# Kernel optimization log

Measured on AMD Instinct MI355X. Metric: run time of the kernel, lower is better.

## Reference

```python
import jax, jax.numpy as jnp
import numpy as np

KV_SIZE = 512


def setup_inputs() -> dict:
    key = jax.random.key(0)
    k1, k2, k3 = jax.random.split(key, 3)
    B, T, C = 8, 4096, 1024
    x = jax.random.normal(k1, (B, T, C), dtype=jnp.float32)
    k_t_1 = jax.random.normal(k2, (B, KV_SIZE, C), dtype=jnp.float32)
    v_t_1 = jax.random.normal(k3, (B, KV_SIZE, C), dtype=jnp.float32)
    return {"x": x, "k_t_1": k_t_1, "v_t_1": v_t_1}


def reference(x, k_t_1, v_t_1):
    # x: [B, T, C]; latent state k_t_1, v_t_1: [B, S=512, C]
    B, T, C = x.shape
    scale = 1.0 / jnp.sqrt(jnp.asarray(C, dtype=x.dtype))

    # Read: queries (tokens) attend over the fixed-size latent KV state.
    scores = jnp.einsum("btc,bsc->bts", x, k_t_1) * scale      # [B, T, S]
    att = jnp.einsum("bts,bsc->btc", jax.nn.softmax(scores, axis=-1), v_t_1)

    # Update: each latent slot attends over the incoming tokens and
    # accumulates the summary into the state (fixed-size KV cache update).
    k_scores = jnp.einsum("bsc,btc->bst", k_t_1, x) * scale     # [B, S, T]
    k_t = k_t_1 + jnp.einsum("bst,btc->bsc", jax.nn.softmax(k_scores, axis=-1), x)
    v_scores = jnp.einsum("bsc,btc->bst", v_t_1, x) * scale     # [B, S, T]
    v_t = v_t_1 + jnp.einsum("bst,btc->bsc", jax.nn.softmax(v_scores, axis=-1), x)

    return att, k_t, v_t
```

## Files before the change

### kernel.cpp

```cpp
#include <hip/hip_runtime.h>
#include <hip/hip_bf16.h>

#define BB 8
#define TT 4096
#define CC 1024
#define SS 512

typedef __bf16 bf16x8 __attribute__((ext_vector_type(8)));
typedef float f32x4 __attribute__((ext_vector_type(4)));
typedef unsigned short u16x8 __attribute__((ext_vector_type(8)));

__device__ __forceinline__ float bf2f(unsigned short u) {
  union { unsigned int i; float f; } x; x.i = ((unsigned int)u) << 16; return x.f;
}
__device__ __forceinline__ unsigned short f2bf(float f) {
  __hip_bfloat16 h = __float2bfloat16(f);
  unsigned short u; __builtin_memcpy(&u, &h, 2); return u;
}

__global__ void cvt_transpose(const float* __restrict__ in,
                              unsigned short* __restrict__ out_rm,
                              unsigned short* __restrict__ out_t,
                              int R, int Cd) {
  __shared__ float tile[64][65];
  const long bo = (long)blockIdx.z * R * Cd;
  const int r0 = blockIdx.x * 64, c0 = blockIdx.y * 64;
  const int tx = threadIdx.x, ty = threadIdx.y;
#pragma unroll
  for (int i = 0; i < 16; ++i) {
    int r = ty + i * 4;
    float v = in[bo + (long)(r0 + r) * Cd + c0 + tx];
    tile[r][tx] = v;
    out_rm[bo + (long)(r0 + r) * Cd + c0 + tx] = f2bf(v);
  }
  if (out_t != nullptr) {
    __syncthreads();
#pragma unroll
    for (int i = 0; i < 16; ++i) {
      int c = ty + i * 4;
      out_t[bo + (long)(c0 + c) * R + r0 + tx] = f2bf(tile[tx][c]);
    }
  }
}

__global__ void transpose_bf16(const unsigned short* __restrict__ in,
                               unsigned short* __restrict__ out,
                               int Rin, int Cin) {
  __shared__ unsigned short tile[64][72];
  const long bo = (long)blockIdx.z * Rin * Cin;
  const int r0 = blockIdx.x * 64, c0 = blockIdx.y * 64;
  const int tid = threadIdx.x;
  const int lr = tid >> 3;
  const int lc = (tid & 7) * 8;
#pragma unroll
  for (int p = 0; p < 2; ++p) {
    int r = lr + p * 32;
    *(u16x8*)&tile[r][lc] = *(const u16x8*)&in[bo + (long)(r0 + r) * Cin + c0 + lc];
  }
  __syncthreads();
#pragma unroll
  for (int p = 0; p < 2; ++p) {
    int s = lr + p * 32;
    u16x8 val;
#pragma unroll
    for (int j = 0; j < 8; ++j) val[j] = tile[lc + j][s];
    *(u16x8*)&out[bo + (long)(c0 + s) * Rin + r0 + lc] = val;
  }
}

template <int ROWLEN>
__global__ __launch_bounds__(256) void row_softmax(unsigned short* __restrict__ sc) {
  constexpr int NV = ROWLEN / 512;
  const int lane = threadIdx.x & 63;
  const long row = (long)blockIdx.x * 4 + (threadIdx.x >> 6);
  unsigned short* base = sc + row * (long)ROWLEN;
  u16x8 d[NV];
  float m = -1e30f;
#pragma unroll
  for (int v = 0; v < NV; ++v) {
    d[v] = *(const u16x8*)&base[(v * 64 + lane) * 8];
#pragma unroll
    for (int j = 0; j < 8; ++j) m = fmaxf(m, bf2f(d[v][j]));
  }
#pragma unroll
  for (int off = 32; off >= 1; off >>= 1) m = fmaxf(m, __shfl_xor(m, off, 64));
  float l = 0.f;
#pragma unroll
  for (int v = 0; v < NV; ++v) {
#pragma unroll
    for (int j = 0; j < 8; ++j) {
      float e = __expf(bf2f(d[v][j]) - m);
      l += e;
      d[v][j] = f2bf(e);
    }
  }
#pragma unroll
  for (int off = 32; off >= 1; off >>= 1) l += __shfl_xor(l, off, 64);
  const float inv = 1.f / l;
#pragma unroll
  for (int v = 0; v < NV; ++v) {
    u16x8 o;
#pragma unroll
    for (int j = 0; j < 8; ++j) o[j] = f2bf(bf2f(d[v][j]) * inv);
    *(u16x8*)&base[(v * 64 + lane) * 8] = o;
  }
}

template <bool OUT_BF16, bool RESID>
__global__ __launch_bounds__(256) void gemm_bt(
    const unsigned short* __restrict__ A, int lda, long sA,
    const unsigned short* __restrict__ Bt, int ldb, long sB,
    void* __restrict__ Cout, int ldc, long sC,
    const float* __restrict__ resid, long sR,
    float alpha, int M, int N, int K) {
  __shared__ unsigned short As[128 * 64];
  __shared__ unsigned short Bs[128 * 64];
  const int zb = blockIdx.z;
  const unsigned short* Ab = A + (long)zb * sA;
  const unsigned short* Bb = Bt + (long)zb * sB;
  const int m0 = blockIdx.y * 128;
  const int n0 = blockIdx.x * 128;
  const int tid = threadIdx.x;
  const int lane = tid & 63;
  const int wm = (tid >> 6) & 1;
  const int wn = tid >> 7;
  const int srow = tid >> 3;
  const int scol = (tid & 7) * 8;
  f32x4 zero = {0.f, 0.f, 0.f, 0.f};
  f32x4 acc[4][4];
#pragma unroll
  for (int i = 0; i < 4; ++i)
#pragma unroll
    for (int j = 0; j < 4; ++j) acc[i][j] = zero;

  for (int k0 = 0; k0 < K; k0 += 64) {
#pragma unroll
    for (int p = 0; p < 4; ++p) {
      int r = srow + p * 32;
      const unsigned short* g = Ab + (long)(m0 + r) * lda + k0 + scol;
      __builtin_amdgcn_global_load_lds(
          (const __attribute__((address_space(1))) void*)g,
          (__attribute__((address_space(3))) void*)&As[r * 64 + scol], 16, 0, 0);
    }
#pragma unroll
    for (int p = 0; p < 4; ++p) {
      int r = srow + p * 32;
      const unsigned short* g = Bb + (long)(n0 + r) * ldb + k0 + scol;
      __builtin_amdgcn_global_load_lds(
          (const __attribute__((address_space(1))) void*)g,
          (__attribute__((address_space(3))) void*)&Bs[r * 64 + scol], 16, 0, 0);
    }
    __syncthreads();
#pragma unroll
    for (int kk = 0; kk < 2; ++kk) {
      const int kof = kk * 32 + (lane >> 4) * 8;
      bf16x8 af[4], bfr[4];
#pragma unroll
      for (int i = 0; i < 4; ++i)
        af[i] = *(const bf16x8*)&As[(wm * 64 + i * 16 + (lane & 15)) * 64 + kof];
#pragma unroll
      for (int j = 0; j < 4; ++j)
        bfr[j] = *(const bf16x8*)&Bs[(wn * 64 + j * 16 + (lane & 15)) * 64 + kof];
#pragma unroll
      for (int i = 0; i < 4; ++i)
#pragma unroll
        for (int j = 0; j < 4; ++j)
          acc[i][j] = __builtin_amdgcn_mfma_f32_16x16x32_bf16(af[i], bfr[j], acc[i][j], 0, 0, 0);
    }
    __syncthreads();
  }
  const int rbase = (lane >> 4) * 4;
  const int cl = lane & 15;
#pragma unroll
  for (int i = 0; i < 4; ++i)
#pragma unroll
    for (int j = 0; j < 4; ++j)
#pragma unroll
      for (int r = 0; r < 4; ++r) {
        int row = m0 + wm * 64 + i * 16 + rbase + r;
        int col = n0 + wn * 64 + j * 16 + cl;
        long idx = (long)row * ldc + col;
        float v = acc[i][j][r] * alpha;
        if (RESID) v += resid[(long)zb * sR + idx];
        if (OUT_BF16)
          ((unsigned short*)Cout)[(long)zb * sC + idx] = f2bf(v);
        else
          ((float*)Cout)[(long)zb * sC + idx] = v;
      }
}

extern "C" void kernel_launch(void* const* d_in, const int* in_sizes, int n_in,
                              void* d_out, int out_size, void* d_ws, size_t ws_size,
                              hipStream_t stream) {
  const float* x = (const float*)d_in[0];
  const float* kin = (const float*)d_in[1];
  const float* vin = (const float*)d_in[2];

  float* att = (float*)d_out;
  float* kt = att + (long)BB * TT * CC;
  float* vt = kt + (long)BB * SS * CC;

  unsigned short* xb = (unsigned short*)d_out;
  unsigned short* xT = xb + (long)BB * TT * CC;

  char* w = (char*)d_ws;
  unsigned short* kb = (unsigned short*)w; w += (long)BB * SS * CC * 2;
  unsigned short* vb = (unsigned short*)w; w += (long)BB * SS * CC * 2;
  unsigned short* vT = (unsigned short*)w; w += (long)BB * CC * SS * 2;
  unsigned short* sc = (unsigned short*)w; w += (long)BB * TT * SS * 2;
  unsigned short* pk = (unsigned short*)w; w += (long)BB * SS * TT * 2;

  const float scale = 0.03125f;
  dim3 cblk(64, 4);

  cvt_transpose<<<dim3(TT / 64, CC / 64, BB), cblk, 0, stream>>>(x, xb, xT, TT, CC);
  cvt_transpose<<<dim3(SS / 64, CC / 64, BB), cblk, 0, stream>>>(kin, kb, (unsigned short*)nullptr, SS, CC);
  cvt_transpose<<<dim3(SS / 64, CC / 64, BB), cblk, 0, stream>>>(vin, vb, vT, SS, CC);

  gemm_bt<true, false><<<dim3(SS / 128, TT / 128, BB), 256, 0, stream>>>(
      xb, CC, (long)TT * CC, kb, CC, (long)SS * CC, sc, SS, (long)TT * SS,
      nullptr, 0, scale, TT, SS, CC);

  transpose_bf16<<<dim3(TT / 64, SS / 64, BB), 256, 0, stream>>>(sc, pk, TT, SS);
  row_softmax<TT><<<BB * SS / 4, 256, 0, stream>>>(pk);

  gemm_bt<false, true><<<dim3(CC / 128, SS / 128, BB), 256, 0, stream>>>(
      pk, TT, (long)SS * TT, xT, TT, (long)CC * TT, kt, CC, (long)SS * CC,
      kin, (long)SS * CC, 1.f, SS, CC, TT);

  row_softmax<SS><<<BB * TT / 4, 256, 0, stream>>>(sc);

  gemm_bt<true, false><<<dim3(TT / 128, SS / 128, BB), 256, 0, stream>>>(
      vb, CC, (long)SS * CC, xb, CC, (long)TT * CC, pk, TT, (long)SS * TT,
      nullptr, 0, scale, SS, TT, CC);
  row_softmax<TT><<<BB * SS / 4, 256, 0, stream>>>(pk);

  gemm_bt<false, true><<<dim3(CC / 128, SS / 128, BB), 256, 0, stream>>>(
      pk, TT, (long)SS * TT, xT, TT, (long)CC * TT, vt, CC, (long)SS * CC,
      vin, (long)SS * CC, 1.f, SS, CC, TT);

  gemm_bt<false, false><<<dim3(CC / 128, TT / 128, BB), 256, 0, stream>>>(
      sc, SS, (long)TT * SS, vT, SS, (long)CC * SS, att, CC, (long)TT * CC,
      nullptr, 0, 1.f, TT, CC, SS);
}
```

Measured before the change: 717.5 us.

## Split-K the state-update GEMMs with atomic accumulation and vectorize conversion transposes

The two update GEMMs (S=512 x C=1024, K=4096) launched only 256 blocks. They now split K four ways across the grid and accumulate with float atomicAdd into outputs pre-seeded with the residual state by a new copy kernel. This is meant to fill the GPU's compute units on these long-K GEMMs, at the cost of extra atomic traffic, two copy kernels and non-deterministic summation order. Separately, the fp32-to-bf16 convert/transpose kernel now uses 256 threads with 16-byte vector loads and stores.

```diff
diff --git a/kernel.cpp b/kernel.cpp
--- a/kernel.cpp
+++ b/kernel.cpp
@@ -8,6 +8,7 @@
 
 typedef __bf16 bf16x8 __attribute__((ext_vector_type(8)));
 typedef float f32x4 __attribute__((ext_vector_type(4)));
+typedef float f32x2 __attribute__((ext_vector_type(2)));
 typedef unsigned short u16x8 __attribute__((ext_vector_type(8)));
 
 __device__ __forceinline__ float bf2f(unsigned short u) {
@@ -22,23 +23,38 @@
                               unsigned short* __restrict__ out_rm,
                               unsigned short* __restrict__ out_t,
                               int R, int Cd) {
-  __shared__ float tile[64][65];
+  __shared__ float tile[64][66];
   const long bo = (long)blockIdx.z * R * Cd;
   const int r0 = blockIdx.x * 64, c0 = blockIdx.y * 64;
-  const int tx = threadIdx.x, ty = threadIdx.y;
-#pragma unroll
-  for (int i = 0; i < 16; ++i) {
-    int r = ty + i * 4;
-    float v = in[bo + (long)(r0 + r) * Cd + c0 + tx];
-    tile[r][tx] = v;
-    out_rm[bo + (long)(r0 + r) * Cd + c0 + tx] = f2bf(v);
+  const int tid = threadIdx.x;
+  const int lr = tid >> 3;
+  const int lc = (tid & 7) * 8;
+#pragma unroll
+  for (int p = 0; p < 2; ++p) {
+    int r = lr + p * 32;
+    const float* src = &in[bo + (long)(r0 + r) * Cd + c0 + lc];
+    f32x4 a = *(const f32x4*)src;
+    f32x4 b = *(const f32x4*)(src + 4);
+    u16x8 o;
+#pragma unroll
+    for (int j = 0; j < 4; ++j) { o[j] = f2bf(a[j]); o[j + 4] = f2bf(b[j]); }
+    *(u16x8*)&out_rm[bo + (long)(r0 + r) * Cd + c0 + lc] = o;
+    if (out_t != nullptr) {
+      *(f32x2*)&tile[r][lc + 0] = f32x2{a[0], a[1]};
+      *(f32x2*)&tile[r][lc + 2] = f32x2{a[2], a[3]};
+      *(f32x2*)&tile[r][lc + 4] = f32x2{b[0], b[1]};
+      *(f32x2*)&tile[r][lc + 6] = f32x2{b[2], b[3]};
+    }
   }
   if (out_t != nullptr) {
     __syncthreads();
 #pragma unroll
-    for (int i = 0; i < 16; ++i) {
-      int c = ty + i * 4;
-      out_t[bo + (long)(c0 + c) * R + r0 + tx] = f2bf(tile[tx][c]);
+    for (int p = 0; p < 2; ++p) {
+      int cc = lr + p * 32;
+      u16x8 val;
+#pragma unroll
+      for (int j = 0; j < 8; ++j) val[j] = f2bf(tile[lc + j][cc]);
+      *(u16x8*)&out_t[bo + (long)(c0 + cc) * R + r0 + lc] = val;
     }
   }
 }
@@ -68,6 +84,11 @@
   }
 }
 
+__global__ void copyf(const float* __restrict__ src, float* __restrict__ dst) {
+  long i = ((long)blockIdx.x * 256 + threadIdx.x) * 4;
+  *(f32x4*)&dst[i] = *(const f32x4*)&src[i];
+}
+
 template <int ROWLEN>
 __global__ __launch_bounds__(256) void row_softmax(unsigned short* __restrict__ sc) {
   constexpr int NV = ROWLEN / 512;
@@ -106,7 +127,7 @@
   }
 }
 
-template <bool OUT_BF16, bool RESID>
+template <bool OUT_BF16, bool RESID, bool ATOMIC, int NSPLIT>
 __global__ __launch_bounds__(256) void gemm_bt(
     const unsigned short* __restrict__ A, int lda, long sA,
     const unsigned short* __restrict__ Bt, int ldb, long sB,
@@ -115,7 +136,9 @@
     float alpha, int M, int N, int K) {
   __shared__ unsigned short As[128 * 64];
   __shared__ unsigned short Bs[128 * 64];
-  const int zb = blockIdx.z;
+  const int zb = blockIdx.z / NSPLIT;
+  const int split = blockIdx.z % NSPLIT;
+  const int Kc = K / NSPLIT;
   const unsigned short* Ab = A + (long)zb * sA;
   const unsigned short* Bb = Bt + (long)zb * sB;
   const int m0 = blockIdx.y * 128;
@@ -133,7 +156,8 @@
 #pragma unroll
     for (int j = 0; j < 4; ++j) acc[i][j] = zero;
 
-  for (int k0 = 0; k0 < K; k0 += 64) {
+  const int kend = (split + 1) * Kc;
+  for (int k0 = split * Kc; k0 < kend; k0 += 64) {
 #pragma unroll
     for (int p = 0; p < 4; ++p) {
       int r = srow + p * 32;
@@ -182,7 +206,9 @@
         long idx = (long)row * ldc + col;
         float v = acc[i][j][r] * alpha;
         if (RESID) v += resid[(long)zb * sR + idx];
-        if (OUT_BF16)
+        if (ATOMIC)
+          atomicAdd(&((float*)Cout)[(long)zb * sC + idx], v);
+        else if (OUT_BF16)
           ((unsigned short*)Cout)[(long)zb * sC + idx] = f2bf(v);
         else
           ((float*)Cout)[(long)zb * sC + idx] = v;
@@ -211,35 +237,37 @@
   unsigned short* pk = (unsigned short*)w; w += (long)BB * SS * TT * 2;
 
   const float scale = 0.03125f;
-  dim3 cblk(64, 4);
-
-  cvt_transpose<<<dim3(TT / 64, CC / 64, BB), cblk, 0, stream>>>(x, xb, xT, TT, CC);
-  cvt_transpose<<<dim3(SS / 64, CC / 64, BB), cblk, 0, stream>>>(kin, kb, (unsigned short*)nullptr, SS, CC);
-  cvt_transpose<<<dim3(SS / 64, CC / 64, BB), cblk, 0, stream>>>(vin, vb, vT, SS, CC);
-
-  gemm_bt<true, false><<<dim3(SS / 128, TT / 128, BB), 256, 0, stream>>>(
+
+  cvt_transpose<<<dim3(TT / 64, CC / 64, BB), 256, 0, stream>>>(x, xb, xT, TT, CC);
+  cvt_transpose<<<dim3(SS / 64, CC / 64, BB), 256, 0, stream>>>(kin, kb, (unsigned short*)nullptr, SS, CC);
+  cvt_transpose<<<dim3(SS / 64, CC / 64, BB), 256, 0, stream>>>(vin, vb, vT, SS, CC);
+
+  copyf<<<(BB * SS * CC) / 1024, 256, 0, stream>>>(kin, kt);
+  copyf<<<(BB * SS * CC) / 1024, 256, 0, stream>>>(vin, vt);
+
+  gemm_bt<true, false, false, 1><<<dim3(SS / 128, TT / 128, BB), 256, 0, stream>>>(
       xb, CC, (long)TT * CC, kb, CC, (long)SS * CC, sc, SS, (long)TT * SS,
       nullptr, 0, scale, TT, SS, CC);
 
   transpose_bf16<<<dim3(TT / 64, SS / 64, BB), 256, 0, stream>>>(sc, pk, TT, SS);
   row_softmax<TT><<<BB * SS / 4, 256, 0, stream>>>(pk);
 
-  gemm_bt<false, true><<<dim3(CC / 128, SS / 128, BB), 256, 0, stream>>>(
+  gemm_bt<false, false, true, 4><<<dim3(CC / 128, SS / 128, BB * 4), 256, 0, stream>>>(
       pk, TT, (long)SS * TT, xT, TT, (long)CC * TT, kt, CC, (long)SS * CC,
-      kin, (long)SS * CC, 1.f, SS, CC, TT);
+      nullptr, 0, 1.f, SS, CC, TT);
 
   row_softmax<SS><<<BB * TT / 4, 256, 0, stream>>>(sc);
 
-  gemm_bt<true, false><<<dim3(TT / 128, SS / 128, BB), 256, 0, stream>>>(
+  gemm_bt<true, false, false, 1><<<dim3(TT / 128, SS / 128, BB), 256, 0, stream>>>(
       vb, CC, (long)SS * CC, xb, CC, (long)TT * CC, pk, TT, (long)SS * TT,
       nullptr, 0, scale, SS, TT, CC);
   row_softmax<TT><<<BB * SS / 4, 256, 0, stream>>>(pk);
 
-  gemm_bt<false, true><<<dim3(CC / 128, SS / 128, BB), 256, 0, stream>>>(
+  gemm_bt<false, false, true, 4><<<dim3(CC / 128, SS / 128, BB * 4), 256, 0, stream>>>(
       pk, TT, (long)SS * TT, xT, TT, (long)CC * TT, vt, CC, (long)SS * CC,
-      vin, (long)SS * CC, 1.f, SS, CC, TT);
-
-  gemm_bt<false, false><<<dim3(CC / 128, TT / 128, BB), 256, 0, stream>>>(
+      nullptr, 0, 1.f, SS, CC, TT);
+
+  gemm_bt<false, false, false, 1><<<dim3(CC / 128, TT / 128, BB), 256, 0, stream>>>(
       sc, SS, (long)TT * SS, vT, SS, (long)CC * SS, att, CC, (long)TT * CC,
       nullptr, 0, 1.f, TT, CC, SS);
 }
```

Measured after the change: 738.6 us. 1.03x slower.
